# Kernel tuning notes

Hardware: AMD Instinct MI355X
Metric: run time of the kernel (lower is better)

## Reference

```python
import jax, jax.numpy as jnp
import numpy as np

N_E = 200000   # number of entities
N_T = 1000000  # number of KB triples
N_R = 200      # number of relations
N_W2V = 300    # question embedding dim
B = 64         # batch size


def _one_step(x, r, subj, rel, obj):
    # torch.sparse.mm(M_subj, x.T)      -> gather: x[:, subj]  (B, N_T)
    # torch.sparse.mm(M_rel.T, r.T)     -> gather: r[:, rel]   (B, N_T)
    # torch.sparse.mm(M_obj.T, x_t*r_t) -> scatter-add over obj ids
    m = x[:, subj] * r[:, rel]                                   # (B, N_T)
    x_new = jax.ops.segment_sum(m.T, obj, num_segments=N_E).T    # (B, N_E)
    return x_new


def setup_inputs() -> dict:
    key = jax.random.key(0)
    ks = jax.random.split(key, 11)
    x = jax.random.uniform(ks[0], (B, N_E), dtype=jnp.float32)
    q = jax.random.normal(ks[1], (B, N_W2V), dtype=jnp.float32)
    subj = jax.random.randint(ks[2], (N_T,), 0, N_E, dtype=jnp.int32)
    rel = jax.random.randint(ks[3], (N_T,), 0, N_R, dtype=jnp.int32)
    obj = jax.random.randint(ks[4], (N_T,), 0, N_E, dtype=jnp.int32)
    s = 1.0 / np.sqrt(N_W2V)  # nn.Linear default init scale
    W1 = jax.random.uniform(ks[5], (N_W2V, N_R), minval=-s, maxval=s, dtype=jnp.float32)
    b1 = jax.random.uniform(ks[6], (N_R,), minval=-s, maxval=s, dtype=jnp.float32)
    W2 = jax.random.uniform(ks[7], (N_W2V, N_R), minval=-s, maxval=s, dtype=jnp.float32)
    b2 = jax.random.uniform(ks[8], (N_R,), minval=-s, maxval=s, dtype=jnp.float32)
    W3 = jax.random.uniform(ks[9], (N_W2V, N_R), minval=-s, maxval=s, dtype=jnp.float32)
    b3 = jax.random.uniform(ks[10], (N_R,), minval=-s, maxval=s, dtype=jnp.float32)
    return {"x": x, "q": q, "W1": W1, "b1": b1, "W2": W2, "b2": b2,
            "W3": W3, "b3": b3, "subj": subj, "rel": rel, "obj": obj,
            "n_hop": 3}


def reference(x, q, W1, b1, W2, b2, W3, b3, subj, rel, obj, n_hop):
    layers = [(W1, b1), (W2, b2), (W3, b3)]
    for W, b in layers[:n_hop]:
        r = q @ W + b              # dense_i(q): (B, N_R)
        x = _one_step(x, r, subj, rel, obj)
    return x
```

## Files before the change

kernel.cpp:

```cpp
#include <hip/hip_runtime.h>
#include <hip/hip_fp16.h>

#define WAVE 64
#define NXCD 8
#define NRMAX 200
#define RSTRIDE 17
#define HOP_TPB 1024
#define HOP_BLOCKS 512
#define CSR_BLOCKS 2048
#define CAP 16
#define OVF_CAP 32768

typedef int v4i __attribute__((ext_vector_type(4)));

__global__ void fused_front_kernel(const float* __restrict__ x, const float* __restrict__ q,
                                   const float* __restrict__ W1, const float* __restrict__ b1,
                                   const float* __restrict__ W2, const float* __restrict__ b2,
                                   const float* __restrict__ W3, const float* __restrict__ b3,
                                   const int* __restrict__ subj, const int* __restrict__ rel,
                                   const int* __restrict__ obj,
                                   int* __restrict__ cnt, unsigned* __restrict__ slots,
                                   int* __restrict__ novf, int* __restrict__ ovf_obj,
                                   unsigned* __restrict__ ovf_pk,
                                   float* __restrict__ rT, __half2* __restrict__ xT,
                                   int N_E, int N_R, int N_W2V, int nT,
                                   int tgrid, int nrx) {
    __shared__ float tile[64][65];
    int bid = blockIdx.x;
    if (bid < CSR_BLOCKS) {
        int grp = bid & (NXCD - 1);
        int sh  = (N_E + NXCD - 1) / NXCD;
        int lo  = grp * sh;
        int hi  = min(N_E, lo + sh);
        int tid    = (bid >> 3) * blockDim.x + threadIdx.x;
        int stride = (CSR_BLOCKS >> 3) * blockDim.x;
        int nT4 = nT >> 2;
        const v4i* obj4 = (const v4i*)obj;
        for (int t = tid; t < nT4; t += stride) {
            v4i o = obj4[t];
            int base = t * 4;
            #pragma unroll
            for (int u = 0; u < 4; ++u) {
                int oo = o[u];
                if (oo >= lo && oo < hi) {
                    unsigned pk = (unsigned)subj[base + u] | ((unsigned)rel[base + u] << 18);
                    int slot = atomicAdd(&cnt[oo], 1);
                    if (slot < CAP) slots[(size_t)oo * CAP + slot] = pk;
                    else {
                        int oi = atomicAdd(novf, 1);
                        if (oi < OVF_CAP) { ovf_obj[oi] = oo; ovf_pk[oi] = pk; }
                    }
                }
            }
        }
        for (int t = nT4 * 4 + tid; t < nT; t += stride) {
            int oo = obj[t];
            if (oo >= lo && oo < hi) {
                unsigned pk = (unsigned)subj[t] | ((unsigned)rel[t] << 18);
                int slot = atomicAdd(&cnt[oo], 1);
                if (slot < CAP) slots[(size_t)oo * CAP + slot] = pk;
                else {
                    int oi = atomicAdd(novf, 1);
                    if (oi < OVF_CAP) { ovf_obj[oi] = oo; ovf_pk[oi] = pk; }
                }
            }
        }
    } else if (bid < CSR_BLOCKS + tgrid) {
        int e0 = (bid - CSR_BLOCKS) * 64;
        int li = threadIdx.x & 63;
        int lo = threadIdx.x >> 6;
        #pragma unroll
        for (int k = 0; k < 16; ++k) {
            int b = lo + 4 * k;
            int e = e0 + li;
            tile[b][li] = (e < N_E) ? x[(size_t)b * N_E + e] : 0.0f;
        }
        __syncthreads();
        #pragma unroll
        for (int k = 0; k < 8; ++k) {
            int idx = k * 256 + threadIdx.x;
            int ei  = idx >> 5;
            int j   = idx & 31;
            int e   = e0 + ei;
            if (e < N_E)
                xT[(size_t)e * 32 + j] = __floats2half2_rn(tile[2 * j][ei], tile[2 * j + 1][ei]);
        }
    } else {
        int rb = bid - CSR_BLOCKS - tgrid;
        int bx = rb % nrx;
        int by = rb / nrx;
        int lane = threadIdx.x & 63;
        int wv   = threadIdx.x >> 6;
        int b    = by * 4 + wv;
        int it   = bx * 64 + lane;
        if (it >= 3 * N_R) return;
        int l = it / N_R;
        int j = it - l * N_R;
        const float* W  = (l == 0) ? W1 : (l == 1) ? W2 : W3;
        const float* bv = (l == 0) ? b1 : (l == 1) ? b2 : b3;
        const float* qrow = q + (size_t)b * N_W2V;
        float a0 = 0.f, a1 = 0.f, a2 = 0.f, a3 = 0.f;
        int k = 0;
        for (; k + 4 <= N_W2V; k += 4) {
            a0 = fmaf(qrow[k + 0], W[(size_t)(k + 0) * N_R + j], a0);
            a1 = fmaf(qrow[k + 1], W[(size_t)(k + 1) * N_R + j], a1);
            a2 = fmaf(qrow[k + 2], W[(size_t)(k + 2) * N_R + j], a2);
            a3 = fmaf(qrow[k + 3], W[(size_t)(k + 3) * N_R + j], a3);
        }
        for (; k < N_W2V; ++k)
            a0 = fmaf(qrow[k], W[(size_t)k * N_R + j], a0);
        rT[(size_t)it * WAVE + b] = bv[j] + ((a0 + a1) + (a2 + a3));
    }
}


__device__ __forceinline__ float4 h4_to_f4(uint2 v) {
    float2 f0 = __half22float2(*(__half2*)&v.x);
    float2 f1 = __half22float2(*(__half2*)&v.y);
    return make_float4(f0.x, f0.y, f1.x, f1.y);
}

__device__ __forceinline__ uint2 pack_half4(float4 a) {
    __half2 h0 = __floats2half2_rn(a.x, a.y);
    __half2 h1 = __floats2half2_rn(a.z, a.w);
    uint2 v;
    v.x = *(unsigned*)&h0;
    v.y = *(unsigned*)&h1;
    return v;
}

__device__ __forceinline__ float4 hop_accum4(const uint2* __restrict__ xp,
                                             const float4* __restrict__ r_lds,
                                             const int* __restrict__ cnt,
                                             const unsigned* __restrict__ slots,
                                             const int* __restrict__ novf,
                                             const int* __restrict__ ovf_obj,
                                             const unsigned* __restrict__ ovf_pk,
                                             int e, int g, int c, int nE) {
    float4 acc = make_float4(0.f, 0.f, 0.f, 0.f);
    int lraw = (e < nE) ? cnt[e] : 0;
    int len = min(lraw, CAP);
    unsigned pv = (c < len) ? slots[(size_t)e * CAP + c] : 0u;
    int m = max(len, __shfl_xor(len, 16));
    m = max(m, __shfl_xor(m, 32));
    for (int j0 = 0; j0 < m; j0 += 8) {
        uint2 xv[8];
        unsigned pr[8];
        #pragma unroll
        for (int u = 0; u < 8; ++u) {
            int jj = max(min(j0 + u, len - 1), 0);
            unsigned p = __shfl(pv, (g << 4) + jj);
            pr[u] = p >> 18;
            xv[u] = xp[(size_t)(p & 0x3FFFFu) * 16 + c];
        }
        #pragma unroll
        for (int u = 0; u < 8; ++u) {
            if (j0 + u < len) {
                float4 rv = r_lds[pr[u] * RSTRIDE + c];
                float4 xf = h4_to_f4(xv[u]);
                acc.x = fmaf(xf.x, rv.x, acc.x);
                acc.y = fmaf(xf.y, rv.y, acc.y);
                acc.z = fmaf(xf.z, rv.z, acc.z);
                acc.w = fmaf(xf.w, rv.w, acc.w);
            }
        }
    }
    if (__any(lraw > CAP)) {
        if (lraw > CAP) {
            int n = min(*novf, OVF_CAP);
            for (int i = 0; i < n; ++i) {
                if (ovf_obj[i] == e) {
                    unsigned p = ovf_pk[i];
                    float4 xf = h4_to_f4(xp[(size_t)(p & 0x3FFFFu) * 16 + c]);
                    float4 rv = r_lds[(p >> 18) * RSTRIDE + c];
                    acc.x = fmaf(xf.x, rv.x, acc.x);
                    acc.y = fmaf(xf.y, rv.y, acc.y);
                    acc.z = fmaf(xf.z, rv.z, acc.z);
                    acc.w = fmaf(xf.w, rv.w, acc.w);
                }
            }
        }
    }
    return acc;
}

__global__ __launch_bounds__(HOP_TPB, 8)
void hop_mid_kernel(const uint2* __restrict__ xp, const float4* __restrict__ rT4,
                    const int* __restrict__ cnt, const unsigned* __restrict__ slots,
                    const int* __restrict__ novf, const int* __restrict__ ovf_obj,
                    const unsigned* __restrict__ ovf_pk,
                    uint2* __restrict__ yh, int nE, int nR) {
    __shared__ float4 r_lds[NRMAX * RSTRIDE];
    for (int i = threadIdx.x; i < nR * 16; i += HOP_TPB)
        r_lds[(i >> 4) * RSTRIDE + (i & 15)] = rT4[i];
    __syncthreads();
    int lane = threadIdx.x & 63;
    int g = lane >> 4, c = lane & 15;
    int wv = threadIdx.x >> 6;
    int nTiles = (nE + 63) >> 6;
    for (int t = blockIdx.x; t < nTiles; t += gridDim.x) {
        int e = t * 64 + wv * 4 + g;
        float4 acc = hop_accum4(xp, r_lds, cnt, slots, novf, ovf_obj, ovf_pk, e, g, c, nE);
        if (e < nE) yh[(size_t)e * 16 + c] = pack_half4(acc);
    }
}

__global__ __launch_bounds__(HOP_TPB, 8)
void hop_out_kernel(const uint2* __restrict__ xp, const float4* __restrict__ rT4,
                    const int* __restrict__ cnt, const unsigned* __restrict__ slots,
                    const int* __restrict__ novf, const int* __restrict__ ovf_obj,
                    const unsigned* __restrict__ ovf_pk,
                    float* __restrict__ out, int nE, int nR) {
    __shared__ float4 r_lds[NRMAX * RSTRIDE];
    __shared__ float tile[64][65];
    for (int i = threadIdx.x; i < nR * 16; i += HOP_TPB)
        r_lds[(i >> 4) * RSTRIDE + (i & 15)] = rT4[i];
    __syncthreads();
    int lane = threadIdx.x & 63;
    int g = lane >> 4, c = lane & 15;
    int wv = threadIdx.x >> 6;
    int nTiles = (nE + 63) >> 6;
    for (int t = blockIdx.x; t < nTiles; t += gridDim.x) {
        int e0 = t * 64;
        int ei = wv * 4 + g;
        float4 acc = hop_accum4(xp, r_lds, cnt, slots, novf, ovf_obj, ovf_pk, e0 + ei, g, c, nE);
        tile[ei][4 * c + 0] = acc.x;
        tile[ei][4 * c + 1] = acc.y;
        tile[ei][4 * c + 2] = acc.z;
        tile[ei][4 * c + 3] = acc.w;
        __syncthreads();
        #pragma unroll
        for (int k = 0; k < 4; ++k) {
            int b = wv * 4 + k;
            int e = e0 + lane;
            if (e < nE) out[(size_t)b * nE + e] = tile[lane][b];
        }
        __syncthreads();
    }
}

extern "C" void kernel_launch(void* const* d_in, const int* in_sizes, int n_in,
                              void* d_out, int out_size, void* d_ws, size_t ws_size,
                              hipStream_t stream) {
    const float* x  = (const float*)d_in[0];
    const float* q  = (const float*)d_in[1];
    const float* W1 = (const float*)d_in[2];
    const float* b1 = (const float*)d_in[3];
    const float* W2 = (const float*)d_in[4];
    const float* b2 = (const float*)d_in[5];
    const float* W3 = (const float*)d_in[6];
    const float* b3 = (const float*)d_in[7];
    const int* subj = (const int*)d_in[8];
    const int* rel  = (const int*)d_in[9];
    const int* obj  = (const int*)d_in[10];

    const int B     = 64;
    const int N_E   = in_sizes[0] / B;
    const int N_W2V = in_sizes[1] / B;
    const int N_R   = in_sizes[3];
    const int N_T   = in_sizes[8];

    const size_t h16bytes = (size_t)N_E * B * sizeof(__half);

    int*      cnt     = (int*)d_ws;
    int*      novf    = cnt + N_E;
    int*      ovf_obj = novf + 4;
    unsigned* ovf_pk  = (unsigned*)(ovf_obj + OVF_CAP);
    unsigned* slots   = ovf_pk + OVF_CAP;
    char*     rT_raw  = (char*)(slots + (size_t)N_E * CAP);
    float*    rT      = (float*)(((uintptr_t)rT_raw + 15) & ~(uintptr_t)15);
    char*     X0      = (char*)(rT + (size_t)3 * N_R * B);
    size_t used = (size_t)(X0 - (char*)d_ws) + h16bytes;

    char* H1;
    if (ws_size >= used + h16bytes) {
        H1 = X0 + h16bytes;
        used += h16bytes;
    } else {
        H1 = (char*)d_out;
    }
    char* H2 = X0;

    hipMemsetAsync(cnt, 0, (size_t)(N_E + 4) * sizeof(int), stream);
    int tgrid = (N_E + 63) / 64;
    int nrx   = (3 * N_R + 63) / 64;
    int rblocks = nrx * (B / 4);
    fused_front_kernel<<<CSR_BLOCKS + tgrid + rblocks, 256, 0, stream>>>(
        x, q, W1, b1, W2, b2, W3, b3, subj, rel, obj,
        cnt, slots, novf, ovf_obj, ovf_pk, rT, (__half2*)X0,
        N_E, N_R, N_W2V, N_T, tgrid, nrx);

    int hblocks = tgrid < HOP_BLOCKS ? tgrid : HOP_BLOCKS;
    const float4* rT1 = (const float4*)rT;
    const float4* rT2 = (const float4*)(rT + (size_t)1 * N_R * B);
    const float4* rT3 = (const float4*)(rT + (size_t)2 * N_R * B);

    hop_mid_kernel<<<hblocks, HOP_TPB, 0, stream>>>(
        (const uint2*)X0, rT1, cnt, slots, novf, ovf_obj, ovf_pk, (uint2*)H1, N_E, N_R);
    hop_mid_kernel<<<hblocks, HOP_TPB, 0, stream>>>(
        (const uint2*)H1, rT2, cnt, slots, novf, ovf_obj, ovf_pk, (uint2*)H2, N_E, N_R);
    hop_out_kernel<<<hblocks, HOP_TPB, 0, stream>>>(
        (const uint2*)H2, rT3, cnt, slots, novf, ovf_obj, ovf_pk, (float*)d_out, N_E, N_R);
}
```

Baseline: 337.9 us.

## Split CSR scatter from prologue and fold counter zeroing into prologue kernel

Moves the counter memset into the prologue kernel, which also does the x transpose and the r projection, and pulls the CSR bucket scatter out into its own kernel launched afterwards. This drops the separate memset call. The cost is that the scatter no longer runs alongside the transpose and matmul blocks in one launch. The scatter cannot start until the prologue finishes, because it must see the zeroed counters.

After: 326.9 us. -3.3%, faster.

```diff
diff --git a/kernel.cpp b/kernel.cpp
--- a/kernel.cpp
+++ b/kernel.cpp
@@ -8,65 +8,23 @@
 #define HOP_TPB 1024
 #define HOP_BLOCKS 512
 #define CSR_BLOCKS 2048
+#define CSR_TPB 256
 #define CAP 16
 #define OVF_CAP 32768
 
 typedef int v4i __attribute__((ext_vector_type(4)));
 
-__global__ void fused_front_kernel(const float* __restrict__ x, const float* __restrict__ q,
-                                   const float* __restrict__ W1, const float* __restrict__ b1,
-                                   const float* __restrict__ W2, const float* __restrict__ b2,
-                                   const float* __restrict__ W3, const float* __restrict__ b3,
-                                   const int* __restrict__ subj, const int* __restrict__ rel,
-                                   const int* __restrict__ obj,
-                                   int* __restrict__ cnt, unsigned* __restrict__ slots,
-                                   int* __restrict__ novf, int* __restrict__ ovf_obj,
-                                   unsigned* __restrict__ ovf_pk,
-                                   float* __restrict__ rT, __half2* __restrict__ xT,
-                                   int N_E, int N_R, int N_W2V, int nT,
-                                   int tgrid, int nrx) {
+__global__ void prologue_kernel(const float* __restrict__ x, const float* __restrict__ q,
+                                const float* __restrict__ W1, const float* __restrict__ b1,
+                                const float* __restrict__ W2, const float* __restrict__ b2,
+                                const float* __restrict__ W3, const float* __restrict__ b3,
+                                float* __restrict__ rT, __half2* __restrict__ xT,
+                                int* __restrict__ cnt, int N_E, int N_R, int N_W2V,
+                                int tgrid, int nrx, int rblocks, int zcount) {
     __shared__ float tile[64][65];
     int bid = blockIdx.x;
-    if (bid < CSR_BLOCKS) {
-        int grp = bid & (NXCD - 1);
-        int sh  = (N_E + NXCD - 1) / NXCD;
-        int lo  = grp * sh;
-        int hi  = min(N_E, lo + sh);
-        int tid    = (bid >> 3) * blockDim.x + threadIdx.x;
-        int stride = (CSR_BLOCKS >> 3) * blockDim.x;
-        int nT4 = nT >> 2;
-        const v4i* obj4 = (const v4i*)obj;
-        for (int t = tid; t < nT4; t += stride) {
-            v4i o = obj4[t];
-            int base = t * 4;
-            #pragma unroll
-            for (int u = 0; u < 4; ++u) {
-                int oo = o[u];
-                if (oo >= lo && oo < hi) {
-                    unsigned pk = (unsigned)subj[base + u] | ((unsigned)rel[base + u] << 18);
-                    int slot = atomicAdd(&cnt[oo], 1);
-                    if (slot < CAP) slots[(size_t)oo * CAP + slot] = pk;
-                    else {
-                        int oi = atomicAdd(novf, 1);
-                        if (oi < OVF_CAP) { ovf_obj[oi] = oo; ovf_pk[oi] = pk; }
-                    }
-                }
-            }
-        }
-        for (int t = nT4 * 4 + tid; t < nT; t += stride) {
-            int oo = obj[t];
-            if (oo >= lo && oo < hi) {
-                unsigned pk = (unsigned)subj[t] | ((unsigned)rel[t] << 18);
-                int slot = atomicAdd(&cnt[oo], 1);
-                if (slot < CAP) slots[(size_t)oo * CAP + slot] = pk;
-                else {
-                    int oi = atomicAdd(novf, 1);
-                    if (oi < OVF_CAP) { ovf_obj[oi] = oo; ovf_pk[oi] = pk; }
-                }
-            }
-        }
-    } else if (bid < CSR_BLOCKS + tgrid) {
-        int e0 = (bid - CSR_BLOCKS) * 64;
+    if (bid < tgrid) {
+        int e0 = bid * 64;
         int li = threadIdx.x & 63;
         int lo = threadIdx.x >> 6;
         #pragma unroll
@@ -85,8 +43,8 @@
             if (e < N_E)
                 xT[(size_t)e * 32 + j] = __floats2half2_rn(tile[2 * j][ei], tile[2 * j + 1][ei]);
         }
-    } else {
-        int rb = bid - CSR_BLOCKS - tgrid;
+    } else if (bid < tgrid + rblocks) {
+        int rb = bid - tgrid;
         int bx = rb % nrx;
         int by = rb / nrx;
         int lane = threadIdx.x & 63;
@@ -110,6 +68,54 @@
         for (; k < N_W2V; ++k)
             a0 = fmaf(qrow[k], W[(size_t)k * N_R + j], a0);
         rT[(size_t)it * WAVE + b] = bv[j] + ((a0 + a1) + (a2 + a3));
+    } else {
+        int zb = bid - tgrid - rblocks;
+        int i4 = zb * 256 + threadIdx.x;
+        if (i4 < zcount) ((v4i*)cnt)[i4] = (v4i){0, 0, 0, 0};
+    }
+}
+
+__global__ void scatter_direct_kernel(const int* __restrict__ subj, const int* __restrict__ rel,
+                                      const int* __restrict__ obj,
+                                      int* __restrict__ cnt, unsigned* __restrict__ slots,
+                                      int* __restrict__ novf, int* __restrict__ ovf_obj,
+                                      unsigned* __restrict__ ovf_pk, int nT, int nE) {
+    int grp = blockIdx.x & (NXCD - 1);
+    int sh  = (nE + NXCD - 1) / NXCD;
+    int lo  = grp * sh;
+    int hi  = min(nE, lo + sh);
+    int tid    = (blockIdx.x >> 3) * blockDim.x + threadIdx.x;
+    int stride = (gridDim.x >> 3) * blockDim.x;
+    int nT4 = nT >> 2;
+    const v4i* obj4 = (const v4i*)obj;
+    for (int t = tid; t < nT4; t += stride) {
+        v4i o = obj4[t];
+        int base = t * 4;
+        #pragma unroll
+        for (int u = 0; u < 4; ++u) {
+            int oo = o[u];
+            if (oo >= lo && oo < hi) {
+                unsigned pk = (unsigned)subj[base + u] | ((unsigned)rel[base + u] << 18);
+                int slot = atomicAdd(&cnt[oo], 1);
+                if (slot < CAP) slots[(size_t)oo * CAP + slot] = pk;
+                else {
+                    int oi = atomicAdd(novf, 1);
+                    if (oi < OVF_CAP) { ovf_obj[oi] = oo; ovf_pk[oi] = pk; }
+                }
+            }
+        }
+    }
+    for (int t = nT4 * 4 + tid; t < nT; t += stride) {
+        int oo = obj[t];
+        if (oo >= lo && oo < hi) {
+            unsigned pk = (unsigned)subj[t] | ((unsigned)rel[t] << 18);
+            int slot = atomicAdd(&cnt[oo], 1);
+            if (slot < CAP) slots[(size_t)oo * CAP + slot] = pk;
+            else {
+                int oi = atomicAdd(novf, 1);
+                if (oi < OVF_CAP) { ovf_obj[oi] = oo; ovf_pk[oi] = pk; }
+            }
+        }
     }
 }
 
@@ -281,14 +287,17 @@
     }
     char* H2 = X0;
 
-    hipMemsetAsync(cnt, 0, (size_t)(N_E + 4) * sizeof(int), stream);
-    int tgrid = (N_E + 63) / 64;
-    int nrx   = (3 * N_R + 63) / 64;
+    int tgrid   = (N_E + 63) / 64;
+    int nrx     = (3 * N_R + 63) / 64;
     int rblocks = nrx * (B / 4);
-    fused_front_kernel<<<CSR_BLOCKS + tgrid + rblocks, 256, 0, stream>>>(
-        x, q, W1, b1, W2, b2, W3, b3, subj, rel, obj,
-        cnt, slots, novf, ovf_obj, ovf_pk, rT, (__half2*)X0,
-        N_E, N_R, N_W2V, N_T, tgrid, nrx);
+    int zcount  = (N_E + 4) / 4;
+    int zblocks = (zcount + 255) / 256;
+    prologue_kernel<<<tgrid + rblocks + zblocks, 256, 0, stream>>>(
+        x, q, W1, b1, W2, b2, W3, b3, rT, (__half2*)X0, cnt,
+        N_E, N_R, N_W2V, tgrid, nrx, rblocks, zcount);
+
+    scatter_direct_kernel<<<CSR_BLOCKS, CSR_TPB, 0, stream>>>(
+        subj, rel, obj, cnt, slots, novf, ovf_obj, ovf_pk, N_T, N_E);
 
     int hblocks = tgrid < HOP_BLOCKS ? tgrid : HOP_BLOCKS;
     const float4* rT1 = (const float4*)rT;
```
